# Kernel tuning notes

Hardware: AMD Instinct MI355X
Metric: run time of the kernel (lower is better)

Reference implementation:

```python
import jax, jax.numpy as jnp
from jax import lax
import numpy as np

L_BANDS = 28
H = 1024
W = 1024


def setup_inputs() -> dict:
    key = jax.random.key(0)
    k1, k2 = jax.random.split(key)
    x_1lhw = jax.random.uniform(k1, (1, L_BANDS, H, W), dtype=jnp.float32)
    mask2d = jax.random.uniform(k2, (H, W), dtype=jnp.float32)
    phi_d_deg = jnp.ones((1,), dtype=jnp.float32)  # dispersion axis angle in degrees
    s_nom = 2.0 * jnp.arange(L_BANDS, dtype=jnp.float32)  # 2 px/band nominal dispersion
    return {"x_1lhw": x_1lhw, "mask2d": mask2d, "phi_d_deg": phi_d_deg, "s_nom": s_nom}


def _int_offsets(phi_d_deg, s_nom):
    # Mirrors torch: offsets come from .item() => detached constants.
    phi = float(np.asarray(phi_d_deg).reshape(())) * np.pi / 180.0
    s = np.asarray(s_nom, dtype=np.float64)
    dx = s * np.cos(phi)
    dy = s * np.sin(phi)
    dx = dx - dx.min()
    dy = dy - dy.min()
    return np.rint(dx).astype(np.int32), np.rint(dy).astype(np.int32)


def reference(x_1lhw, mask2d, phi_d_deg, s_nom):
    _, L, Hh, Ww = x_1lhw.shape
    dx_i, dy_i = _int_offsets(phi_d_deg, s_nom)
    Hp = Hh + int(dy_i.max())
    Wp = Ww + int(dx_i.max())
    bands = mask2d[None, :, :] * x_1lhw[0]  # [L, H, W] coded bands

    def step(y, inp):
        band, oy, ox = inp
        patch = lax.dynamic_slice(y, (oy, ox), (Hh, Ww)) + band
        return lax.dynamic_update_slice(y, patch, (oy, ox)), None

    y0 = jnp.zeros((Hp, Wp), dtype=x_1lhw.dtype)
    y, _ = lax.scan(step, y0, (bands, jnp.asarray(dy_i), jnp.asarray(dx_i)))
    return y[None]  # [1, Hp, Wp]
```

## Files before the change

### kernel.cpp

```cpp
#include <hip/hip_runtime.h>
#include <math.h>

#define NL 28
#define H 1024
#define W 1024
#define HW (H * W)
#define GB 4
#define NG 7
#define BROW 1152
#define GUARD 64

typedef float f2 __attribute__((ext_vector_type(2), aligned(4)));

typedef __attribute__((address_space(1))) const void GV;
typedef __attribute__((address_space(3))) void LV;
__device__ __forceinline__ void gl_lds16(const float* g, float* l) {
    __builtin_amdgcn_global_load_lds((GV*)g, (LV*)l, 16, 0, 0);
}

__global__ __launch_bounds__(256)
void cassi_v8(const float* __restrict__ x, const float* __restrict__ mask,
              const float* __restrict__ phi_deg, const float* __restrict__ s_nom,
              float* __restrict__ out, int out_size)
{
    __shared__ float xbuf[2][GB][BROW];
    __shared__ float mbuf[2][BROW];
    __shared__ int s_dx[NL], s_dy[NL];
    __shared__ unsigned s_pk[NL];
    __shared__ int s_geom[4];

    const int tid = threadIdx.x;
    const int lane = tid & 63;
    const int wid = tid >> 6;

    if (tid < 64) {
        float phi = phi_deg[0] * 0.017453292519943295f;
        float c = cosf(phi), sn = sinf(phi);
        float s = (tid < NL) ? s_nom[tid] : 0.f;
        float dxv = s * c, dyv = s * sn;
        float dxm = (tid < NL) ? dxv : 3.0e38f;
        float dym = (tid < NL) ? dyv : 3.0e38f;
        for (int d = 1; d < 64; d <<= 1) {
            dxm = fminf(dxm, __shfl_xor(dxm, d, 64));
            dym = fminf(dym, __shfl_xor(dym, d, 64));
        }
        int dxi = (tid < NL) ? (int)rintf(dxv - dxm) : 0;
        int dyi = (tid < NL) ? (int)rintf(dyv - dym) : 0;
        int dxmax = dxi, dymax = dyi;
        for (int d = 1; d < 64; d <<= 1) {
            dxmax = max(dxmax, __shfl_xor(dxmax, d, 64));
            dymax = max(dymax, __shfl_xor(dymax, d, 64));
        }
        if (tid < NL) {
            s_dx[tid] = dxi;
            s_dy[tid] = dyi;
            int moff = dyi * BROW + GUARD - dxi;
            s_pk[tid] = ((unsigned)moff << 16) | (unsigned)(GUARD - dxi);
        }
        if (tid == 0) {
            int Wp = W + dxmax;
            s_geom[0] = Wp;
            s_geom[1] = out_size / Wp;
            s_geom[2] = dxmax;
            s_geom[3] = dymax;
        }
    }
    __syncthreads();

    const int Wp = s_geom[0], Hp = s_geom[1];
    const int Y = blockIdx.x;
    const bool fast = (s_geom[3] <= 1) && (s_geom[2] <= GUARD);

    if (!fast) {
        for (int i = blockIdx.x * 256 + tid; i < out_size; i += gridDim.x * 256) {
            int Yk = i / Wp, Xk = i - Yk * Wp;
            float a = 0.f;
            for (int l = 0; l < NL; ++l) {
                int h = Yk - s_dy[l], w = Xk - s_dx[l];
                if ((unsigned)h < (unsigned)H && (unsigned)w < (unsigned)W) {
                    int p = h * W + w;
                    a = fmaf(mask[p], x[(size_t)l * HW + p], a);
                }
            }
            out[i] = a;
        }
        return;
    }
    if (Y >= Hp) return;

    unsigned pk[NL];
#pragma unroll
    for (int l = 0; l < NL; ++l) pk[l] = s_pk[l];

    if (wid < 2) {
        int g = Y - wid;
        float* dst = &mbuf[wid][GUARD];
        if ((unsigned)g < (unsigned)H) {
            const float* src = mask + (size_t)g * W + lane * 4;
            gl_lds16(src, dst);
            gl_lds16(src + 256, dst + 256);
            gl_lds16(src + 512, dst + 512);
            gl_lds16(src + 768, dst + 768);
        } else {
            for (int k = lane; k < 1024; k += 64) dst[k] = 0.f;
        }
    }
    {
        int r = tid >> 7, c0 = tid & 127;
        int c = (c0 < GUARD) ? c0 : (1024 + c0);
        mbuf[r][c] = 0.f;
    }
    {
        int dy = s_dy[wid];
        int srow = min(max(Y - dy, 0), H - 1);
        const float* src = x + (size_t)wid * HW + (size_t)srow * W + lane * 4;
        float* dst = &xbuf[0][wid][GUARD];
        gl_lds16(src, dst);
        gl_lds16(src + 256, dst + 256);
        gl_lds16(src + 512, dst + 512);
        gl_lds16(src + 768, dst + 768);
    }
    __syncthreads();

    int Xe0 = (2 * tid + 1 < Wp) ? 2 * tid : 0;
    int Xe1 = (2 * tid + 512 + 1 < Wp) ? 2 * tid + 512 : 0;
    int Xe2 = (2 * tid + 1024 + 1 < Wp) ? 2 * tid + 1024 : 0;

    f2 acc0 = {0.f, 0.f}, acc1 = {0.f, 0.f}, acc2 = {0.f, 0.f};
    const float* xf = &xbuf[0][0][0];
    const float* mf = &mbuf[0][0];

#pragma unroll
    for (int g = 0; g < NG; ++g) {
        if (g < NG - 1) {
            int l = (g + 1) * GB + wid;
            int dy = s_dy[l];
            int srow = min(max(Y - dy, 0), H - 1);
            const float* src = x + (size_t)l * HW + (size_t)srow * W + lane * 4;
            float* dst = &xbuf[(g + 1) & 1][wid][GUARD];
            gl_lds16(src, dst);
            gl_lds16(src + 256, dst + 256);
            gl_lds16(src + 512, dst + 512);
            gl_lds16(src + 768, dst + 768);
        }
#pragma unroll
        for (int w = 0; w < GB; ++w) {
            const int l = g * GB + w;
            unsigned p = pk[l];
            const int xo = (int)(p & 0xffffu) + ((g & 1) * GB + w) * BROW;
            const int mo = (int)(p >> 16);
            {
                f2 xv = *(const f2*)&xf[xo + Xe0];
                f2 mv = *(const f2*)&mf[mo + Xe0];
                acc0 += xv * mv;
            }
            {
                f2 xv = *(const f2*)&xf[xo + Xe1];
                f2 mv = *(const f2*)&mf[mo + Xe1];
                acc1 += xv * mv;
            }
            {
                f2 xv = *(const f2*)&xf[xo + Xe2];
                f2 mv = *(const f2*)&mf[mo + Xe2];
                acc2 += xv * mv;
            }
        }
        asm volatile("s_waitcnt vmcnt(0)" ::: "memory");
        __builtin_amdgcn_s_barrier();
    }

    float* orow = out + (size_t)Y * Wp;
    {
        int X = 2 * tid;
        if (X + 1 < Wp) *(f2*)(orow + X) = acc0;
        else if (X < Wp) orow[X] = acc0.x;
    }
    {
        int X = 2 * tid + 512;
        if (X + 1 < Wp) *(f2*)(orow + X) = acc1;
        else if (X < Wp) orow[X] = acc1.x;
    }
    {
        int X = 2 * tid + 1024;
        if (X + 1 < Wp) *(f2*)(orow + X) = acc2;
        else if (X < Wp) orow[X] = acc2.x;
    }
}

extern "C" void kernel_launch(void* const* d_in, const int* in_sizes, int n_in,
                              void* d_out, int out_size, void* d_ws, size_t ws_size,
                              hipStream_t stream) {
    const float* x = (const float*)d_in[0];
    const float* mask = (const float*)d_in[1];
    const float* phi = (const float*)d_in[2];
    const float* s_nom = (const float*)d_in[3];
    float* out = (float*)d_out;

    const int blocks = out_size / W + 2;
    cassi_v8<<<blocks, 256, 0, stream>>>(x, mask, phi, s_nom, out, out_size);
}
```

Measured before the change: 31.34 us.

## Triple-buffer band row loads to prefetch two groups ahead

Moves from double to triple buffering of the x band rows in LDS, issuing async global-to-LDS loads two groups ahead and waiting with vmcnt(4) so one group's loads stay in flight across each barrier. The aim is to hide global memory latency better in this bandwidth-bound accumulate kernel. It also zeroes the guard columns of all x buffers explicitly. The cost is more LDS per block, which may lower occupancy.

```diff
diff --git a/kernel.cpp b/kernel.cpp
--- a/kernel.cpp
+++ b/kernel.cpp
@@ -7,6 +7,7 @@
 #define HW (H * W)
 #define GB 4
 #define NG 7
+#define NBUF 3
 #define BROW 1152
 #define GUARD 64
 
@@ -19,11 +20,11 @@
 }
 
 __global__ __launch_bounds__(256)
-void cassi_v8(const float* __restrict__ x, const float* __restrict__ mask,
-              const float* __restrict__ phi_deg, const float* __restrict__ s_nom,
-              float* __restrict__ out, int out_size)
+void cassi_v10(const float* __restrict__ x, const float* __restrict__ mask,
+               const float* __restrict__ phi_deg, const float* __restrict__ s_nom,
+               float* __restrict__ out, int out_size)
 {
-    __shared__ float xbuf[2][GB][BROW];
+    __shared__ float xbuf[NBUF][GB][BROW];
     __shared__ float mbuf[2][BROW];
     __shared__ int s_dx[NL], s_dy[NL];
     __shared__ unsigned s_pk[NL];
@@ -92,6 +93,17 @@
 #pragma unroll
     for (int l = 0; l < NL; ++l) pk[l] = s_pk[l];
 
+    {
+        float* xflat = &xbuf[0][0][0];
+#pragma unroll
+        for (int j = 0; j < (NBUF * GB * 2 * GUARD) / 256; ++j) {
+            int e = j * 256 + tid;
+            int row = e >> 7;
+            int c0 = e & 127;
+            int c = (c0 < GUARD) ? c0 : (1024 + c0);
+            xflat[row * BROW + c] = 0.f;
+        }
+    }
     if (wid < 2) {
         int g = Y - wid;
         float* dst = &mbuf[wid][GUARD];
@@ -110,17 +122,19 @@
         int c = (c0 < GUARD) ? c0 : (1024 + c0);
         mbuf[r][c] = 0.f;
     }
-    {
-        int dy = s_dy[wid];
-        int srow = min(max(Y - dy, 0), H - 1);
-        const float* src = x + (size_t)wid * HW + (size_t)srow * W + lane * 4;
-        float* dst = &xbuf[0][wid][GUARD];
+#pragma unroll
+    for (int g0 = 0; g0 < 2; ++g0) {
+        int l = g0 * GB + wid;
+        int srow = min(max(Y - s_dy[l], 0), H - 1);
+        const float* src = x + (size_t)l * HW + (size_t)srow * W + lane * 4;
+        float* dst = &xbuf[g0][wid][GUARD];
         gl_lds16(src, dst);
         gl_lds16(src + 256, dst + 256);
         gl_lds16(src + 512, dst + 512);
         gl_lds16(src + 768, dst + 768);
     }
-    __syncthreads();
+    asm volatile("s_waitcnt vmcnt(4) lgkmcnt(0)" ::: "memory");
+    __builtin_amdgcn_s_barrier();
 
     int Xe0 = (2 * tid + 1 < Wp) ? 2 * tid : 0;
     int Xe1 = (2 * tid + 512 + 1 < Wp) ? 2 * tid + 512 : 0;
@@ -132,12 +146,11 @@
 
 #pragma unroll
     for (int g = 0; g < NG; ++g) {
-        if (g < NG - 1) {
-            int l = (g + 1) * GB + wid;
-            int dy = s_dy[l];
-            int srow = min(max(Y - dy, 0), H - 1);
+        if (g + 2 < NG) {
+            int l = (g + 2) * GB + wid;
+            int srow = min(max(Y - s_dy[l], 0), H - 1);
             const float* src = x + (size_t)l * HW + (size_t)srow * W + lane * 4;
-            float* dst = &xbuf[(g + 1) & 1][wid][GUARD];
+            float* dst = &xbuf[(g + 2) % NBUF][wid][GUARD];
             gl_lds16(src, dst);
             gl_lds16(src + 256, dst + 256);
             gl_lds16(src + 512, dst + 512);
@@ -147,7 +160,7 @@
         for (int w = 0; w < GB; ++w) {
             const int l = g * GB + w;
             unsigned p = pk[l];
-            const int xo = (int)(p & 0xffffu) + ((g & 1) * GB + w) * BROW;
+            const int xo = (int)(p & 0xffffu) + ((g % NBUF) * GB + w) * BROW;
             const int mo = (int)(p >> 16);
             {
                 f2 xv = *(const f2*)&xf[xo + Xe0];
@@ -165,8 +178,13 @@
                 acc2 += xv * mv;
             }
         }
-        asm volatile("s_waitcnt vmcnt(0)" ::: "memory");
-        __builtin_amdgcn_s_barrier();
+        if (g + 2 < NG) {
+            asm volatile("s_waitcnt vmcnt(4) lgkmcnt(0)" ::: "memory");
+            __builtin_amdgcn_s_barrier();
+        } else if (g + 1 < NG) {
+            asm volatile("s_waitcnt vmcnt(0) lgkmcnt(0)" ::: "memory");
+            __builtin_amdgcn_s_barrier();
+        }
     }
 
     float* orow = out + (size_t)Y * Wp;
@@ -197,5 +215,5 @@
     float* out = (float*)d_out;
 
     const int blocks = out_size / W + 2;
-    cassi_v8<<<blocks, 256, 0, stream>>>(x, mask, phi, s_nom, out, out_size);
+    cassi_v10<<<blocks, 256, 0, stream>>>(x, mask, phi, s_nom, out, out_size);
 }
```

After: 30.95 us. Within noise of the previous version (-1.2%).

## Give each wave its own band subset with per-wave triple-buffered loads

Applied to the files above, without the earlier changes.

Each of the four waves now owns seven bands and streams them through a private triple-buffered LDS region, waiting on its own vmcnt instead of taking a block-wide barrier per band group. Each wave accumulates the whole output row, and the four partial rows are reduced through LDS at the end. Offset setup moves from a shared-memory broadcast to per-wave shuffles, which removes the initial block barrier. The cost is more accumulator registers and a final LDS reduction.

```diff
diff --git a/kernel.cpp b/kernel.cpp
--- a/kernel.cpp
+++ b/kernel.cpp
@@ -5,10 +5,12 @@
 #define H 1024
 #define W 1024
 #define HW (H * W)
-#define GB 4
-#define NG 7
 #define BROW 1152
 #define GUARD 64
+#define WBANDS 7
+#define NBUF 3
+#define WREG (NBUF * BROW)
+#define NPASS 9
 
 typedef float f2 __attribute__((ext_vector_type(2), aligned(4)));
 
@@ -19,64 +21,45 @@
 }
 
 __global__ __launch_bounds__(256)
-void cassi_v8(const float* __restrict__ x, const float* __restrict__ mask,
-              const float* __restrict__ phi_deg, const float* __restrict__ s_nom,
-              float* __restrict__ out, int out_size)
+void cassi_v11(const float* __restrict__ x, const float* __restrict__ mask,
+               const float* __restrict__ phi_deg, const float* __restrict__ s_nom,
+               float* __restrict__ out, int out_size)
 {
-    __shared__ float xbuf[2][GB][BROW];
-    __shared__ float mbuf[2][BROW];
-    __shared__ int s_dx[NL], s_dy[NL];
-    __shared__ unsigned s_pk[NL];
-    __shared__ int s_geom[4];
+    __shared__ float lds[4 * WREG + 2 * BROW];
 
     const int tid = threadIdx.x;
     const int lane = tid & 63;
     const int wid = tid >> 6;
 
-    if (tid < 64) {
-        float phi = phi_deg[0] * 0.017453292519943295f;
-        float c = cosf(phi), sn = sinf(phi);
-        float s = (tid < NL) ? s_nom[tid] : 0.f;
-        float dxv = s * c, dyv = s * sn;
-        float dxm = (tid < NL) ? dxv : 3.0e38f;
-        float dym = (tid < NL) ? dyv : 3.0e38f;
-        for (int d = 1; d < 64; d <<= 1) {
-            dxm = fminf(dxm, __shfl_xor(dxm, d, 64));
-            dym = fminf(dym, __shfl_xor(dym, d, 64));
-        }
-        int dxi = (tid < NL) ? (int)rintf(dxv - dxm) : 0;
-        int dyi = (tid < NL) ? (int)rintf(dyv - dym) : 0;
-        int dxmax = dxi, dymax = dyi;
-        for (int d = 1; d < 64; d <<= 1) {
-            dxmax = max(dxmax, __shfl_xor(dxmax, d, 64));
-            dymax = max(dymax, __shfl_xor(dymax, d, 64));
-        }
-        if (tid < NL) {
-            s_dx[tid] = dxi;
-            s_dy[tid] = dyi;
-            int moff = dyi * BROW + GUARD - dxi;
-            s_pk[tid] = ((unsigned)moff << 16) | (unsigned)(GUARD - dxi);
-        }
-        if (tid == 0) {
-            int Wp = W + dxmax;
-            s_geom[0] = Wp;
-            s_geom[1] = out_size / Wp;
-            s_geom[2] = dxmax;
-            s_geom[3] = dymax;
-        }
+    float phi = phi_deg[0] * 0.017453292519943295f;
+    float c = cosf(phi), sn = sinf(phi);
+    float s = (lane < NL) ? s_nom[lane] : 0.f;
+    float dxv = s * c, dyv = s * sn;
+    float dxm = (lane < NL) ? dxv : 3.0e38f;
+    float dym = (lane < NL) ? dyv : 3.0e38f;
+    for (int d = 1; d < 64; d <<= 1) {
+        dxm = fminf(dxm, __shfl_xor(dxm, d, 64));
+        dym = fminf(dym, __shfl_xor(dym, d, 64));
     }
-    __syncthreads();
+    int dxi = (lane < NL) ? (int)rintf(dxv - dxm) : 0;
+    int dyi = (lane < NL) ? (int)rintf(dyv - dym) : 0;
+    int dxmax = dxi, dymax = dyi;
+    for (int d = 1; d < 64; d <<= 1) {
+        dxmax = max(dxmax, __shfl_xor(dxmax, d, 64));
+        dymax = max(dymax, __shfl_xor(dymax, d, 64));
+    }
+    const int Wp = W + dxmax;
+    const int Hp = out_size / Wp;
 
-    const int Wp = s_geom[0], Hp = s_geom[1];
-    const int Y = blockIdx.x;
-    const bool fast = (s_geom[3] <= 1) && (s_geom[2] <= GUARD);
-
-    if (!fast) {
+    if (!(dymax <= 1 && dxmax <= GUARD)) {
         for (int i = blockIdx.x * 256 + tid; i < out_size; i += gridDim.x * 256) {
             int Yk = i / Wp, Xk = i - Yk * Wp;
             float a = 0.f;
             for (int l = 0; l < NL; ++l) {
-                int h = Yk - s_dy[l], w = Xk - s_dx[l];
+                float sl = s_nom[l];
+                int dx = (int)rintf(sl * c - dxm);
+                int dy = (int)rintf(sl * sn - dym);
+                int h = Yk - dy, w = Xk - dx;
                 if ((unsigned)h < (unsigned)H && (unsigned)w < (unsigned)W) {
                     int p = h * W + w;
                     a = fmaf(mask[p], x[(size_t)l * HW + p], a);
@@ -86,104 +69,114 @@
         }
         return;
     }
+
+    const int Y = blockIdx.x;
     if (Y >= Hp) return;
 
-    unsigned pk[NL];
+    float* xw = &lds[wid * WREG];
+    float* mb = &lds[4 * WREG];
+
 #pragma unroll
-    for (int l = 0; l < NL; ++l) pk[l] = s_pk[l];
-
+    for (int b = 0; b < NBUF; ++b) {
+        xw[b * BROW + lane] = 0.f;
+        xw[b * BROW + GUARD + 1024 + lane] = 0.f;
+    }
     if (wid < 2) {
         int g = Y - wid;
-        float* dst = &mbuf[wid][GUARD];
+        float* mrow = &mb[wid * BROW];
         if ((unsigned)g < (unsigned)H) {
             const float* src = mask + (size_t)g * W + lane * 4;
-            gl_lds16(src, dst);
-            gl_lds16(src + 256, dst + 256);
-            gl_lds16(src + 512, dst + 512);
-            gl_lds16(src + 768, dst + 768);
+            gl_lds16(src,       mrow + GUARD);
+            gl_lds16(src + 256, mrow + GUARD + 256);
+            gl_lds16(src + 512, mrow + GUARD + 512);
+            gl_lds16(src + 768, mrow + GUARD + 768);
+            mrow[lane] = 0.f;
+            mrow[GUARD + 1024 + lane] = 0.f;
         } else {
-            for (int k = lane; k < 1024; k += 64) dst[k] = 0.f;
+            for (int k = lane; k < BROW; k += 64) mrow[k] = 0.f;
         }
     }
-    {
-        int r = tid >> 7, c0 = tid & 127;
-        int c = (c0 < GUARD) ? c0 : (1024 + c0);
-        mbuf[r][c] = 0.f;
-    }
-    {
-        int dy = s_dy[wid];
-        int srow = min(max(Y - dy, 0), H - 1);
-        const float* src = x + (size_t)wid * HW + (size_t)srow * W + lane * 4;
-        float* dst = &xbuf[0][wid][GUARD];
+#pragma unroll
+    for (int j = 0; j < 2; ++j) {
+        int l = wid * WBANDS + j;
+        int dyj = __shfl(dyi, l, 64);
+        int srow = min(max(Y - dyj, 0), H - 1);
+        const float* src = x + (size_t)l * HW + (size_t)srow * W + lane * 4;
+        float* dst = xw + j * BROW + GUARD;
         gl_lds16(src, dst);
         gl_lds16(src + 256, dst + 256);
         gl_lds16(src + 512, dst + 512);
         gl_lds16(src + 768, dst + 768);
     }
-    __syncthreads();
+    asm volatile("s_waitcnt vmcnt(8) lgkmcnt(0)" ::: "memory");
+    __builtin_amdgcn_s_barrier();
 
-    int Xe0 = (2 * tid + 1 < Wp) ? 2 * tid : 0;
-    int Xe1 = (2 * tid + 512 + 1 < Wp) ? 2 * tid + 512 : 0;
-    int Xe2 = (2 * tid + 1024 + 1 < Wp) ? 2 * tid + 1024 : 0;
+    int te[NPASS];
+#pragma unroll
+    for (int p = 0; p < NPASS; ++p) {
+        int t = p * 128 + 2 * lane;
+        te[p] = (t < Wp) ? t : 0;
+    }
 
-    f2 acc0 = {0.f, 0.f}, acc1 = {0.f, 0.f}, acc2 = {0.f, 0.f};
-    const float* xf = &xbuf[0][0][0];
-    const float* mf = &mbuf[0][0];
+    f2 acc[NPASS];
+#pragma unroll
+    for (int p = 0; p < NPASS; ++p) acc[p] = f2{0.f, 0.f};
 
 #pragma unroll
-    for (int g = 0; g < NG; ++g) {
-        if (g < NG - 1) {
-            int l = (g + 1) * GB + wid;
-            int dy = s_dy[l];
-            int srow = min(max(Y - dy, 0), H - 1);
+    for (int j = 0; j < WBANDS; ++j) {
+        if (j + 2 < WBANDS) {
+            int l = wid * WBANDS + j + 2;
+            int dyj = __shfl(dyi, l, 64);
+            int srow = min(max(Y - dyj, 0), H - 1);
             const float* src = x + (size_t)l * HW + (size_t)srow * W + lane * 4;
-            float* dst = &xbuf[(g + 1) & 1][wid][GUARD];
+            float* dst = xw + ((j + 2) % NBUF) * BROW + GUARD;
             gl_lds16(src, dst);
             gl_lds16(src + 256, dst + 256);
             gl_lds16(src + 512, dst + 512);
             gl_lds16(src + 768, dst + 768);
         }
+        if (j + 2 < WBANDS)      asm volatile("s_waitcnt vmcnt(8)" ::: "memory");
+        else if (j + 1 < WBANDS) asm volatile("s_waitcnt vmcnt(4)" ::: "memory");
+        else                     asm volatile("s_waitcnt vmcnt(0)" ::: "memory");
+
+        int l = wid * WBANDS + j;
+        int dxj = __shfl(dxi, l, 64);
+        int dyj = __shfl(dyi, l, 64);
+        const float* xb = xw + (j % NBUF) * BROW + GUARD - dxj;
+        const float* mrow = mb + dyj * BROW + GUARD - dxj;
 #pragma unroll
-        for (int w = 0; w < GB; ++w) {
-            const int l = g * GB + w;
-            unsigned p = pk[l];
-            const int xo = (int)(p & 0xffffu) + ((g & 1) * GB + w) * BROW;
-            const int mo = (int)(p >> 16);
-            {
-                f2 xv = *(const f2*)&xf[xo + Xe0];
-                f2 mv = *(const f2*)&mf[mo + Xe0];
-                acc0 += xv * mv;
-            }
-            {
-                f2 xv = *(const f2*)&xf[xo + Xe1];
-                f2 mv = *(const f2*)&mf[mo + Xe1];
-                acc1 += xv * mv;
-            }
-            {
-                f2 xv = *(const f2*)&xf[xo + Xe2];
-                f2 mv = *(const f2*)&mf[mo + Xe2];
-                acc2 += xv * mv;
-            }
+        for (int p = 0; p < NPASS; ++p) {
+            f2 xv = *(const f2*)&xb[te[p]];
+            f2 mv = *(const f2*)&mrow[te[p]];
+            acc[p] += xv * mv;
         }
-        asm volatile("s_waitcnt vmcnt(0)" ::: "memory");
-        __builtin_amdgcn_s_barrier();
+        asm volatile("s_waitcnt lgkmcnt(0)" ::: "memory");
+        __builtin_amdgcn_sched_barrier(0);
     }
 
+#pragma unroll
+    for (int p = 0; p < NPASS; ++p) {
+        int t = p * 128 + 2 * lane;
+        if (t + 1 < Wp)      *(f2*)&xw[t] = acc[p];
+        else if (t < Wp)     xw[t] = acc[p].x;
+    }
+    asm volatile("s_waitcnt lgkmcnt(0)" ::: "memory");
+    __builtin_amdgcn_s_barrier();
+
     float* orow = out + (size_t)Y * Wp;
-    {
-        int X = 2 * tid;
-        if (X + 1 < Wp) *(f2*)(orow + X) = acc0;
-        else if (X < Wp) orow[X] = acc0.x;
-    }
-    {
-        int X = 2 * tid + 512;
-        if (X + 1 < Wp) *(f2*)(orow + X) = acc1;
-        else if (X < Wp) orow[X] = acc1.x;
-    }
-    {
-        int X = 2 * tid + 1024;
-        if (X + 1 < Wp) *(f2*)(orow + X) = acc2;
-        else if (X < Wp) orow[X] = acc2.x;
+#pragma unroll
+    for (int q = 0; q < 3; ++q) {
+        int t = 2 * (tid + q * 256);
+        if (t + 1 < Wp) {
+            f2 v = *(const f2*)&lds[0 * WREG + t];
+            v += *(const f2*)&lds[1 * WREG + t];
+            v += *(const f2*)&lds[2 * WREG + t];
+            v += *(const f2*)&lds[3 * WREG + t];
+            *(f2*)&orow[t] = v;
+        } else if (t < Wp) {
+            orow[t] = lds[0 * WREG + t] + lds[1 * WREG + t]
+                    + lds[2 * WREG + t] + lds[3 * WREG + t];
+        }
     }
 }
 
@@ -197,5 +190,5 @@
     float* out = (float*)d_out;
 
     const int blocks = out_size / W + 2;
-    cassi_v8<<<blocks, 256, 0, stream>>>(x, mask, phi, s_nom, out, out_size);
+    cassi_v11<<<blocks, 256, 0, stream>>>(x, mask, phi, s_nom, out, out_size);
 }
```

Result: faster. 28.54 us (-8.9%).
